# Performance work log

Hardware: AMD Instinct MI355X
Metric: run time of the kernel (lower is better)

Reference implementation:

```python
import jax, jax.numpy as jnp
import numpy as np

NEG_SLOPE = 0.2  # GATConv default negative_slope


def gat_conv(x, row, col, W, b, a_src, a_dst, N):
    # GATConv, heads=1, flow='target_to_source': i=row (central), j=col (neighbor)
    h = x @ W                                                   # [N, C]
    e = jax.nn.leaky_relu((h @ a_src)[col] + (h @ a_dst)[row], NEG_SLOPE)  # [E]
    m = jax.ops.segment_max(e, row, num_segments=N)             # segment softmax over row
    w = jnp.exp(e - m[row])
    denom = jax.ops.segment_sum(w, row, num_segments=N)
    alpha = w / (denom[row] + 1e-16)
    out = jax.ops.segment_sum(alpha[:, None] * h[col], row, num_segments=N)
    return out + b


def lstm_scan(xs_t, Wih, Whh, bih, bhh):
    # xs_t: [L, N, C] -> hidden states [L, N, H]; PyTorch gate order i,f,g,o
    H = Whh.shape[1]
    Nn = xs_t.shape[1]
    bias = bih + bhh
    def step(carry, xt):
        h, c = carry
        g = xt @ Wih.T + h @ Whh.T + bias
        i, f, gg, o = jnp.split(g, 4, axis=-1)
        c = jax.nn.sigmoid(f) * c + jax.nn.sigmoid(i) * jnp.tanh(gg)
        h = jax.nn.sigmoid(o) * jnp.tanh(c)
        return (h, c), h
    init = (jnp.zeros((Nn, H), xs_t.dtype), jnp.zeros((Nn, H), xs_t.dtype))
    _, hs = jax.lax.scan(step, init, xs_t)
    return hs


def jk_lstm(xst, Wih_f, Whh_f, bih_f, bhh_f, Wih_b, Whh_b, bih_b, bhh_b, att_W, att_b):
    # xst: [L, N, C]; bidirectional LSTM over layer dim, attention-weighted sum
    hf = lstm_scan(xst, Wih_f, Whh_f, bih_f, bhh_f)
    hb = lstm_scan(xst[::-1], Wih_b, Whh_b, bih_b, bhh_b)[::-1]
    h = jnp.concatenate([hf, hb], axis=-1)                      # [L, N, 2H]
    score = jnp.einsum('lnh,h->ln', h, att_W) + att_b           # [L, N]
    alpha = jax.nn.softmax(score, axis=0)                       # softmax over layers
    return jnp.einsum('lnc,ln->nc', xst, alpha)                 # [N, C]


def setup_inputs() -> dict:
    key = jax.random.key(0)
    ks = list(jax.random.split(key, 32))
    N, E, C = 50000, 800000, 128
    L = 3
    H = (L * C) // 2  # 192; PyG JumpingKnowledge lstm hidden size
    s = 0.05
    d = {}
    d['x'] = jax.random.normal(ks[0], (N, 3), jnp.float32)
    d['edge_index'] = jax.random.randint(ks[1], (2, E), 0, N, jnp.int64)
    d['gat_W0'] = jax.random.normal(ks[2], (3, C)) * 0.3
    d['gat_b0'] = jnp.zeros((C,))
    d['gat_as0'] = jax.random.normal(ks[3], (C,)) * s
    d['gat_ad0'] = jax.random.normal(ks[4], (C,)) * s
    d['gat_W'] = jax.random.normal(ks[5], (L - 1, C, C)) * s
    d['gat_b'] = jnp.zeros((L - 1, C))
    d['gat_as'] = jax.random.normal(ks[6], (L - 1, C)) * s
    d['gat_ad'] = jax.random.normal(ks[7], (L - 1, C)) * s
    d['lstm_Wih_f'] = jax.random.normal(ks[8], (4 * H, C)) * s
    d['lstm_Whh_f'] = jax.random.normal(ks[9], (4 * H, H)) * s
    d['lstm_bih_f'] = jnp.zeros((4 * H,))
    d['lstm_bhh_f'] = jnp.zeros((4 * H,))
    d['lstm_Wih_b'] = jax.random.normal(ks[10], (4 * H, C)) * s
    d['lstm_Whh_b'] = jax.random.normal(ks[11], (4 * H, H)) * s
    d['lstm_bih_b'] = jnp.zeros((4 * H,))
    d['lstm_bhh_b'] = jnp.zeros((4 * H,))
    d['att_W'] = jax.random.normal(ks[12], (2 * H,)) * s
    d['att_b'] = jnp.zeros((1,))
    d['nW1'] = jax.random.normal(ks[13], (C, C)) * s
    d['nb1'] = jnp.zeros((C,))
    d['nW2'] = jax.random.normal(ks[14], (C, 2)) * s
    d['nb2'] = jnp.zeros((2,))
    d['eW1'] = jax.random.normal(ks[15], (2 * C, C)) * s
    d['eb1'] = jnp.zeros((C,))
    d['eW2'] = jax.random.normal(ks[16], (C, 2)) * s
    d['eb2'] = jnp.zeros((2,))
    return d


def reference(x, edge_index, gat_W0, gat_b0, gat_as0, gat_ad0, gat_W, gat_b, gat_as, gat_ad,
              lstm_Wih_f, lstm_Whh_f, lstm_bih_f, lstm_bhh_f,
              lstm_Wih_b, lstm_Whh_b, lstm_bih_b, lstm_bhh_b,
              att_W, att_b, nW1, nb1, nW2, nb2, eW1, eb1, eW2, eb2):
    N = x.shape[0]
    row, col = edge_index[0], edge_index[1]
    xs = []
    h = jax.nn.relu(gat_conv(x, row, col, gat_W0, gat_b0, gat_as0, gat_ad0, N))
    xs.append(h)
    for l in range(gat_W.shape[0]):  # fixed small layer count
        h = jax.nn.relu(gat_conv(h, row, col, gat_W[l], gat_b[l], gat_as[l], gat_ad[l], N))
        xs.append(h)
    xst = jnp.stack(xs, axis=0)  # [L, N, C]
    h = jk_lstm(xst, lstm_Wih_f, lstm_Whh_f, lstm_bih_f, lstm_bhh_f,
                lstm_Wih_b, lstm_Whh_b, lstm_bih_b, lstm_bhh_b, att_W, att_b)
    # node classifier (dropout is identity in eval)
    node_out = jax.nn.softmax(jax.nn.relu(h @ nW1 + nb1) @ nW2 + nb2, axis=1)
    # edge representation gather + concat, then edge classifier
    edge_rep = jnp.concatenate([h[row], h[col]], axis=1)  # [E, 2C]
    edge_out = jax.nn.softmax(jax.nn.relu(edge_rep @ eW1 + eb1) @ eW2 + eb2, axis=1)
    return node_out, edge_out
```

## Files before the change

kernel.cpp:

```cpp
#include <hip/hip_runtime.h>
#include <cstdint>
#include <cstddef>


#define NIN 28
#define MAXJOBS 20

struct InPtrs { const void* p[NIN]; int n[NIN]; };

struct ConvJobs {
    const void* src[MAXJOBS];
    float* dst[MAXJOBS];
    int n[MAXJOBS];
    int ai[MAXJOBS];
    int blk0[MAXJOBS + 1];
    int njobs;
};

typedef short s16x4 __attribute__((ext_vector_type(4)));
typedef short s16x8 __attribute__((ext_vector_type(8)));
typedef float f32x4 __attribute__((ext_vector_type(4)));
typedef unsigned short u16x8 __attribute__((ext_vector_type(8)));

__device__ __forceinline__ float bf2f(unsigned short v) {
    unsigned int u = ((unsigned int)v) << 16;
    return __uint_as_float(u);
}

__device__ __forceinline__ unsigned short f2bf(float x) {
    unsigned int u = __float_as_uint(x);
    unsigned int r = u + 0x7fffu + ((u >> 16) & 1u);
    return (unsigned short)(r >> 16);
}

__device__ __forceinline__ float rdx(const void* p, size_t i, int isf32) {
    return isf32 ? ((const float*)p)[i] : bf2f(((const unsigned short*)p)[i]);
}

__device__ __forceinline__ float frcp(float x) {
    return __builtin_amdgcn_rcpf(x);
}

__device__ __forceinline__ float sigm(float x) {
    return frcp(1.f + __expf(-x));
}

__device__ __forceinline__ float fast_tanh(float x) {
    return 1.f - 2.f * frcp(__expf(2.f * x) + 1.f);
}

__global__ void k_sniff(InPtrs in, int* flags) {
    int ai = blockIdx.x;
    if (ai >= NIN) return;
    __shared__ int cnt;
    if (threadIdx.x == 0) cnt = 0;
    __syncthreads();
    if (ai == 1) {
        const int* w = (const int*)in.p[1];
        int nw = in.n[1] < 512 ? in.n[1] : 512;
        int local = 0;
        for (int i = threadIdx.x; i < nw; i += blockDim.x)
            if ((i & 1) && w[i] != 0) local++;
        atomicAdd(&cnt, local);
        __syncthreads();
        if (threadIdx.x == 0) flags[1] = (cnt < 4) ? 1 : 0;
        return;
    }
    const unsigned short* u = (const unsigned short*)in.p[ai];
    int ns = in.n[ai] < 256 ? in.n[ai] : 256;
    int local = 0;
    for (int i = threadIdx.x; i < ns; i += blockDim.x) {
        if (i & 1) continue;
        unsigned short v = u[i];
        int e = (v >> 7) & 0xff;
        if ((v & 0x7fff) != 0 && (e < 100 || e > 154)) local++;
    }
    atomicAdd(&cnt, local);
    __syncthreads();
    if (threadIdx.x == 0) flags[ai] = (cnt * 4 >= ns) ? 1 : 0;
}

__global__ void k_convall(ConvJobs J, const int* __restrict__ flags) {
    int b = blockIdx.x;
    int j = 0;
    while (j + 1 < J.njobs && b >= J.blk0[j + 1]) ++j;
    int i = (b - J.blk0[j]) * 256 + threadIdx.x;
    if (i >= J.n[j]) return;
    J.dst[j][i] = rdx(J.src[j], i, flags[J.ai[j]]);
}

__global__ void k_conve(const void* src, int* row, int* col, int E, const int* flags) {
    int i = blockIdx.x * blockDim.x + threadIdx.x;
    if (i >= E) return;
    if (flags[1]) {
        const long long* s = (const long long*)src;
        row[i] = (int)s[i];
        col[i] = (int)s[(size_t)E + i];
    } else {
        const int* s = (const int*)src;
        row[i] = s[i];
        col[i] = s[(size_t)E + i];
    }
}

__global__ void k_zeroi(int* p, int n) {
    int i = blockIdx.x * blockDim.x + threadIdx.x;
    if (i < n) p[i] = 0;
}

__global__ void k_hist(const int* __restrict__ row, int* __restrict__ cnt, int E) {
    int i = blockIdx.x * blockDim.x + threadIdx.x;
    if (i < E) atomicAdd(&cnt[row[i]], 1);
}

__global__ void k_scan1(const int* __restrict__ deg, int* __restrict__ indptr,
                        int* __restrict__ bsums, int N) {
    __shared__ int buf[1024];
    const int t = threadIdx.x;
    const int base = blockIdx.x * 1024;
    int v = (base + t < N) ? deg[base + t] : 0;
    buf[t] = v;
    __syncthreads();
    for (int ofs = 1; ofs < 1024; ofs <<= 1) {
        int add = (t >= ofs) ? buf[t - ofs] : 0;
        __syncthreads();
        buf[t] += add;
        __syncthreads();
    }
    if (base + t < N) indptr[base + t] = buf[t] - v;
    if (t == 1023) bsums[blockIdx.x] = buf[1023];
}

__global__ void k_scan2(int* bsums, int nb) {
    if (threadIdx.x == 0 && blockIdx.x == 0) {
        int acc = 0;
        for (int j = 0; j < nb; ++j) { int v = bsums[j]; bsums[j] = acc; acc += v; }
        bsums[nb] = acc;
    }
}

__global__ void k_scan3(const int* __restrict__ bsums, int* __restrict__ indptr,
                        int N, int nb) {
    int i = blockIdx.x * blockDim.x + threadIdx.x;
    if (i < N) indptr[i] += bsums[i >> 10];
    if (i == 0) indptr[N] = bsums[nb];
}

__global__ void k_fill(const int* __restrict__ row, const int* __restrict__ col,
                       const int* __restrict__ indptr, int* __restrict__ cur,
                       int* __restrict__ colS, int E) {
    int i = blockIdx.x * blockDim.x + threadIdx.x;
    if (i >= E) return;
    int r = row[i];
    int p = indptr[r] + atomicAdd(&cur[r], 1);
    colS[p] = col[i];
}

__global__ __launch_bounds__(256) void k_lin0(
    const float* __restrict__ x, const float* __restrict__ W0,
    const float* __restrict__ asrc, const float* __restrict__ adst,
    unsigned short* __restrict__ hlin, float* __restrict__ hs, float* __restrict__ hd,
    int N) {
    const int wid = threadIdx.x >> 6, lane = threadIdx.x & 63;
    const int n = blockIdx.x * 4 + wid;
    if (n >= N) return;
    float x0 = x[(size_t)n * 3], x1 = x[(size_t)n * 3 + 1], x2 = x[(size_t)n * 3 + 2];
    const int c0 = lane, c1 = lane + 64;
    float h0 = x0 * W0[c0] + x1 * W0[128 + c0] + x2 * W0[256 + c0];
    float h1 = x0 * W0[c1] + x1 * W0[128 + c1] + x2 * W0[256 + c1];
    hlin[(size_t)n * 128 + c0] = f2bf(h0);
    hlin[(size_t)n * 128 + c1] = f2bf(h1);
    float sp = h0 * asrc[c0] + h1 * asrc[c1];
    float dp = h0 * adst[c0] + h1 * adst[c1];
    for (int o = 32; o; o >>= 1) { sp += __shfl_down(sp, o); dp += __shfl_down(dp, o); }
    if (lane == 0) { hs[n] = sp; hd[n] = dp; }
}

__global__ __launch_bounds__(256) void k_lin(
    const unsigned short* __restrict__ xin, const float* __restrict__ W,
    const float* __restrict__ asrc, const float* __restrict__ adst,
    unsigned short* __restrict__ hlin, float* __restrict__ hs, float* __restrict__ hd,
    int N) {
    __shared__ float xl[16][128];
    const int t = threadIdx.x;
    const int wid = t >> 6, lane = t & 63;
    const int nb = blockIdx.x * 16;
    for (int i = t; i < 2048; i += 256) {
        int r = i >> 7, k = i & 127;
        int n = nb + r;
        xl[r][k] = (n < N) ? bf2f(xin[(size_t)n * 128 + k]) : 0.f;
    }
    __syncthreads();
    const int c0 = lane, c1 = lane + 64;
    const int r0 = wid * 4;
    float h0[4], h1[4];
    #pragma unroll
    for (int j = 0; j < 4; ++j) { h0[j] = 0.f; h1[j] = 0.f; }
    #pragma unroll 2
    for (int k = 0; k < 128; ++k) {
        float w0 = W[k * 128 + c0], w1 = W[k * 128 + c1];
        #pragma unroll
        for (int j = 0; j < 4; ++j) {
            float xv = xl[r0 + j][k];
            h0[j] += xv * w0;
            h1[j] += xv * w1;
        }
    }
    float sp[4], dp[4];
    #pragma unroll
    for (int j = 0; j < 4; ++j) {
        sp[j] = h0[j] * asrc[c0] + h1[j] * asrc[c1];
        dp[j] = h0[j] * adst[c0] + h1[j] * adst[c1];
    }
    #pragma unroll
    for (int o = 32; o; o >>= 1) {
        #pragma unroll
        for (int j = 0; j < 4; ++j) {
            sp[j] += __shfl_down(sp[j], o);
            dp[j] += __shfl_down(dp[j], o);
        }
    }
    #pragma unroll
    for (int j = 0; j < 4; ++j) {
        int n = nb + r0 + j;
        if (n < N) {
            hlin[(size_t)n * 128 + c0] = f2bf(h0[j]);
            hlin[(size_t)n * 128 + c1] = f2bf(h1[j]);
            if (lane == 0) { hs[n] = sp[j]; hd[n] = dp[j]; }
        }
    }
}

__global__ __launch_bounds__(256) void k_aggr(
    const unsigned short* __restrict__ hlin, const float* __restrict__ hs,
    const float* __restrict__ hd,
    const int* __restrict__ indptr, const int* __restrict__ colS,
    const float* __restrict__ b, unsigned short* __restrict__ xout, int N) {
    const int wid = threadIdx.x >> 6, lane = threadIdx.x & 63;
    const int n = blockIdx.x * 4 + wid;
    if (n >= N) return;
    const int s = indptr[n], epos = indptr[n + 1];
    const float hdv = hd[n];
    const int c0 = lane, c1 = lane + 64;
    float m = -1e30f, d = 0.f, a0 = 0.f, a1 = 0.f;
    int idx = s;
    for (; idx + 8 <= epos; idx += 8) {
        int cl[8];
        #pragma unroll
        for (int j = 0; j < 8; ++j) cl[j] = colS[idx + j];
        float e[8];
        #pragma unroll
        for (int j = 0; j < 8; ++j) {
            float ev = hs[cl[j]] + hdv;
            e[j] = (ev > 0.f) ? ev : 0.2f * ev;
        }
        float v0[8], v1[8];
        #pragma unroll
        for (int j = 0; j < 8; ++j) {
            const unsigned short* hp = hlin + (size_t)cl[j] * 128;
            v0[j] = bf2f(hp[c0]);
            v1[j] = bf2f(hp[c1]);
        }
        float m8 = e[0];
        #pragma unroll
        for (int j = 1; j < 8; ++j) m8 = fmaxf(m8, e[j]);
        if (m8 > m) {
            float sc = __expf(m - m8);
            a0 *= sc; a1 *= sc; d *= sc; m = m8;
        }
        #pragma unroll
        for (int j = 0; j < 8; ++j) {
            float w = __expf(e[j] - m);
            a0 += w * v0[j];
            a1 += w * v1[j];
            d  += w;
        }
    }
    for (; idx < epos; ++idx) {
        int col = colS[idx];
        float e = hs[col] + hdv;
        e = (e > 0.f) ? e : 0.2f * e;
        const unsigned short* hr = hlin + (size_t)col * 128;
        float v0 = bf2f(hr[c0]), v1 = bf2f(hr[c1]);
        if (e > m) {
            float sc = __expf(m - e);
            a0 = a0 * sc + v0;
            a1 = a1 * sc + v1;
            d  = d * sc + 1.f;
            m  = e;
        } else {
            float w = __expf(e - m);
            a0 += w * v0;
            a1 += w * v1;
            d  += w;
        }
    }
    float inv = frcp(d + 1e-16f);
    float r0 = a0 * inv + b[c0];
    float r1 = a1 * inv + b[c1];
    xout[(size_t)n * 128 + c0] = f2bf(fmaxf(r0, 0.f));
    xout[(size_t)n * 128 + c1] = f2bf(fmaxf(r1, 0.f));
}

__global__ void k_wpack(const void* Wihf, const void* Whhf,
                        const void* Wihb, const void* Whhb,
                        const void* bihf, const void* bhhf,
                        const void* bihb, const void* bhhb,
                        const int* __restrict__ flags,
                        unsigned short* __restrict__ Bpack, float* __restrict__ bsum) {
    int idx = blockIdx.x * blockDim.x + threadIdx.x;
    const int TOT = 2 * 10 * 48 * 512;
    if (idx < TOT) {
        int dir = idx / (10 * 48 * 512);
        int r   = idx % (10 * 48 * 512);
        int kb  = r / (48 * 512);
        int r2  = r % (48 * 512);
        int f   = r2 / 512;
        int q   = r2 % 512;
        int lane = q >> 3, j = q & 7;
        int k   = kb * 32 + ((j >> 2) * 16) + ((lane >> 4) * 4) + (j & 3);
        int col = f * 16 + (lane & 15);
        float v;
        if (k < 128)
            v = dir ? rdx(Wihb, (size_t)col * 128 + k, flags[14])
                    : rdx(Wihf, (size_t)col * 128 + k, flags[10]);
        else
            v = dir ? rdx(Whhb, (size_t)col * 192 + (k - 128), flags[15])
                    : rdx(Whhf, (size_t)col * 192 + (k - 128), flags[11]);
        Bpack[idx] = f2bf(v);
    }
    if (idx < 2 * 768) {
        int d = idx / 768, j = idx % 768;
        bsum[idx] = d ? rdx(bihb, j, flags[16]) + rdx(bhhb, j, flags[17])
                      : rdx(bihf, j, flags[12]) + rdx(bhhf, j, flags[13]);
    }
}

__global__ __launch_bounds__(768, 3) void k_lstm_mfma(
    const unsigned short* __restrict__ xsb,
    const unsigned short* __restrict__ Bpack,
    const float* __restrict__ bsum,
    const float* __restrict__ attW,
    float* __restrict__ scoreP,
    int N) {
    __shared__ unsigned short AS[64][332];
    __shared__ float scoreS[64];
    const int t = threadIdx.x;
    const int bf = t >> 6, lane = t & 63;
    const int dir = blockIdx.y;
    const int n0 = blockIdx.x * 64;
    const int ccol = lane & 15;
    const int klane = lane >> 4;
    const int lrow = klane * 4;
    const int akl = klane * 4;
    const int m = bf * 16 + ccol;

    const float bI = bsum[dir * 768 + m];
    const float bF = bsum[dir * 768 + 192 + m];
    const float bG = bsum[dir * 768 + 384 + m];
    const float bO = bsum[dir * 768 + 576 + m];
    const float awt = attW[dir * 192 + m];
    float cst[16];
    #pragma unroll
    for (int i = 0; i < 16; ++i) cst[i] = 0.f;

    const unsigned short* Bd = Bpack + (size_t)dir * 10 * 48 * 512;

    for (int s = 0; s < 3; ++s) {
        const int l = dir ? (2 - s) : s;
        {
            const unsigned short* xsrc = xsb + ((size_t)l * N + n0) * 128;
            for (int i = t; i < 1024; i += 768) {
                int r = i >> 4, kq = (i & 15) * 8;
                u16x8 v = (u16x8)(0);
                if (n0 + r < N) v = *(const u16x8*)(xsrc + (size_t)r * 128 + kq);
                *(u16x8*)&AS[r][kq] = v;
            }
        }
        if (t < 64) scoreS[t] = 0.f;
        __syncthreads();

        const int KB = s ? 10 : 4;
        f32x4 acc[4][4];
        #pragma unroll
        for (int rf = 0; rf < 4; ++rf)
            #pragma unroll
            for (int g = 0; g < 4; ++g) acc[rf][g] = (f32x4)(0.f);
        s16x8 bA[4], bB[4];
        {
            const unsigned short* bb = Bd + (size_t)bf * 512 + lane * 8;
            #pragma unroll
            for (int g = 0; g < 4; ++g) bA[g] = *(const s16x8*)(bb + (size_t)g * 6144);
        }
        for (int kb = 0; kb < KB; kb += 2) {
            {
                const unsigned short* bb = Bd + ((size_t)(kb + 1) * 48 + bf) * 512 + lane * 8;
                #pragma unroll
                for (int g = 0; g < 4; ++g) bB[g] = *(const s16x8*)(bb + (size_t)g * 6144);
            }
            {
                const int k0 = kb * 32 + akl;
                s16x8 av[4];
                #pragma unroll
                for (int rf = 0; rf < 4; ++rf) {
                    s16x4 alo = *(const s16x4*)&AS[rf * 16 + ccol][k0];
                    s16x4 ahi = *(const s16x4*)&AS[rf * 16 + ccol][k0 + 16];
                    av[rf] = __builtin_shufflevector(alo, ahi, 0, 1, 2, 3, 4, 5, 6, 7);
                }
                #pragma unroll
                for (int rf = 0; rf < 4; ++rf)
                    #pragma unroll
                    for (int g = 0; g < 4; ++g)
                        acc[rf][g] = __builtin_amdgcn_mfma_f32_16x16x32_bf16(
                            av[rf], bA[g], acc[rf][g], 0, 0, 0);
            }
            if (kb + 2 < KB) {
                const unsigned short* bb = Bd + ((size_t)(kb + 2) * 48 + bf) * 512 + lane * 8;
                #pragma unroll
                for (int g = 0; g < 4; ++g) bA[g] = *(const s16x8*)(bb + (size_t)g * 6144);
            }
            {
                const int k0 = (kb + 1) * 32 + akl;
                s16x8 av[4];
                #pragma unroll
                for (int rf = 0; rf < 4; ++rf) {
                    s16x4 alo = *(const s16x4*)&AS[rf * 16 + ccol][k0];
                    s16x4 ahi = *(const s16x4*)&AS[rf * 16 + ccol][k0 + 16];
                    av[rf] = __builtin_shufflevector(alo, ahi, 0, 1, 2, 3, 4, 5, 6, 7);
                }
                #pragma unroll
                for (int rf = 0; rf < 4; ++rf)
                    #pragma unroll
                    for (int g = 0; g < 4; ++g)
                        acc[rf][g] = __builtin_amdgcn_mfma_f32_16x16x32_bf16(
                            av[rf], bB[g], acc[rf][g], 0, 0, 0);
            }
        }
        __syncthreads();

        float sp[16];
        #pragma unroll
        for (int rf = 0; rf < 4; ++rf) {
            #pragma unroll
            for (int reg = 0; reg < 4; ++reg) {
                float gI = acc[rf][0][reg] + bI;
                float gF = acc[rf][1][reg] + bF;
                float gG = acc[rf][2][reg] + bG;
                float gO = acc[rf][3][reg] + bO;
                float ig = sigm(gI);
                float fg = sigm(gF);
                float gt = fast_tanh(gG);
                float og = sigm(gO);
                int ci = rf * 4 + reg;
                float cn = fg * cst[ci] + ig * gt;
                cst[ci] = cn;
                float hh = og * fast_tanh(cn);
                AS[rf * 16 + lrow + reg][128 + m] = f2bf(hh);
                sp[ci] = hh * awt;
            }
        }
        #pragma unroll
        for (int o = 1; o < 16; o <<= 1) {
            #pragma unroll
            for (int i = 0; i < 16; ++i) sp[i] += __shfl_xor(sp[i], o);
        }
        if (ccol == 0) {
            #pragma unroll
            for (int i = 0; i < 16; ++i)
                atomicAdd(&scoreS[(i >> 2) * 16 + lrow + (i & 3)], sp[i]);
        }
        __syncthreads();
        if (t < 64 && n0 + t < N)
            scoreP[(size_t)(dir * 3 + l) * N + n0 + t] = scoreS[t];
    }
}

__global__ __launch_bounds__(256) void k_tail(
    const unsigned short* __restrict__ xsb, const float* __restrict__ scoreP,
    const float* __restrict__ nW1, const float* __restrict__ nb1,
    const float* __restrict__ nW2, const float* __restrict__ nb2,
    const float* __restrict__ eW1, const float* __restrict__ eb1,
    unsigned short* __restrict__ P, unsigned short* __restrict__ Q,
    float* __restrict__ out, int N) {
    __shared__ float xl[16][128];
    __shared__ float al[16][4];
    const int t = threadIdx.x;
    const int wid = t >> 6, lane = t & 63;
    const int nb = blockIdx.x * 16;
    if (t < 16) {
        int n = nb + t;
        float e0 = 0.f, e1 = 0.f, e2 = 0.f;
        if (n < N) {
            float s0 = scoreP[n]                 + scoreP[(size_t)3 * N + n];
            float s1 = scoreP[(size_t)N + n]     + scoreP[(size_t)4 * N + n];
            float s2 = scoreP[(size_t)2 * N + n] + scoreP[(size_t)5 * N + n];
            float mm = fmaxf(s0, fmaxf(s1, s2));
            e0 = __expf(s0 - mm); e1 = __expf(s1 - mm); e2 = __expf(s2 - mm);
            float inv = frcp(e0 + e1 + e2);
            e0 *= inv; e1 *= inv; e2 *= inv;
        }
        al[t][0] = e0; al[t][1] = e1; al[t][2] = e2;
    }
    __syncthreads();
    const size_t L1o = (size_t)N * 128, L2o = 2 * L1o;
    for (int i = t; i < 2048; i += 256) {
        int r = i >> 7, k = i & 127;
        int n = nb + r;
        float v = 0.f;
        if (n < N) {
            size_t p = (size_t)n * 128 + k;
            v = al[r][0] * bf2f(xsb[p]) + al[r][1] * bf2f(xsb[L1o + p])
              + al[r][2] * bf2f(xsb[L2o + p]);
        }
        xl[r][k] = v;
    }
    __syncthreads();
    const int c0 = lane, c1 = lane + 64;
    const int r0 = wid * 4;
    {
        float h0[4], h1[4];
        #pragma unroll
        for (int j = 0; j < 4; ++j) { h0[j] = 0.f; h1[j] = 0.f; }
        #pragma unroll 2
        for (int k = 0; k < 128; ++k) {
            float w0 = nW1[k * 128 + c0], w1 = nW1[k * 128 + c1];
            #pragma unroll
            for (int j = 0; j < 4; ++j) {
                float xv = xl[r0 + j][k];
                h0[j] += xv * w0;
                h1[j] += xv * w1;
            }
        }
        float p0[4], p1[4];
        #pragma unroll
        for (int j = 0; j < 4; ++j) {
            float a = fmaxf(h0[j] + nb1[c0], 0.f);
            float bq = fmaxf(h1[j] + nb1[c1], 0.f);
            p0[j] = a * nW2[c0 * 2 + 0] + bq * nW2[c1 * 2 + 0];
            p1[j] = a * nW2[c0 * 2 + 1] + bq * nW2[c1 * 2 + 1];
        }
        #pragma unroll
        for (int o = 32; o; o >>= 1) {
            #pragma unroll
            for (int j = 0; j < 4; ++j) {
                p0[j] += __shfl_down(p0[j], o);
                p1[j] += __shfl_down(p1[j], o);
            }
        }
        if (lane == 0) {
            #pragma unroll
            for (int j = 0; j < 4; ++j) {
                int n = nb + r0 + j;
                if (n < N) {
                    float l0 = p0[j] + nb2[0], l1 = p1[j] + nb2[1];
                    float mm = fmaxf(l0, l1);
                    float e0 = __expf(l0 - mm), e1 = __expf(l1 - mm);
                    float inv = frcp(e0 + e1);
                    out[2 * (size_t)n]     = e0 * inv;
                    out[2 * (size_t)n + 1] = e1 * inv;
                }
            }
        }
    }
    {
        float pp0[4], pp1[4], qq0[4], qq1[4];
        #pragma unroll
        for (int j = 0; j < 4; ++j) { pp0[j] = 0.f; pp1[j] = 0.f; qq0[j] = 0.f; qq1[j] = 0.f; }
        for (int k = 0; k < 128; ++k) {
            float wp0 = eW1[k * 128 + c0], wp1 = eW1[k * 128 + c1];
            float wq0 = eW1[(128 + k) * 128 + c0], wq1 = eW1[(128 + k) * 128 + c1];
            #pragma unroll
            for (int j = 0; j < 4; ++j) {
                float xv = xl[r0 + j][k];
                pp0[j] += xv * wp0; pp1[j] += xv * wp1;
                qq0[j] += xv * wq0; qq1[j] += xv * wq1;
            }
        }
        #pragma unroll
        for (int j = 0; j < 4; ++j) {
            int n = nb + r0 + j;
            if (n < N) {
                P[(size_t)n * 128 + c0] = f2bf(pp0[j] + eb1[c0]);
                P[(size_t)n * 128 + c1] = f2bf(pp1[j] + eb1[c1]);
                Q[(size_t)n * 128 + c0] = f2bf(qq0[j]);
                Q[(size_t)n * 128 + c1] = f2bf(qq1[j]);
            }
        }
    }
}

__global__ __launch_bounds__(256) void k_edge2(
    const unsigned short* __restrict__ P, const unsigned short* __restrict__ Q,
    const int* __restrict__ row, const int* __restrict__ col,
    const float* __restrict__ W2, const float* __restrict__ b2,
    float* __restrict__ out, long long E, int N) {
    long long g = (((long long)blockIdx.x * blockDim.x) + threadIdx.x) >> 4;
    const int sl = threadIdx.x & 15;
    if (g >= E) return;
    int r = row[g], c = col[g];
    u16x8 pv = *(const u16x8*)(P + (size_t)r * 128 + sl * 8);
    u16x8 qv = *(const u16x8*)(Q + (size_t)c * 128 + sl * 8);
    const float4* w2 = (const float4*)W2 + sl * 4;
    float l0 = 0.f, l1 = 0.f;
    #pragma unroll
    for (int jj = 0; jj < 4; ++jj) {
        float h0 = fmaxf(bf2f(pv[2 * jj])     + bf2f(qv[2 * jj]), 0.f);
        float h1 = fmaxf(bf2f(pv[2 * jj + 1]) + bf2f(qv[2 * jj + 1]), 0.f);
        float4 wv = w2[jj];
        l0 += h0 * wv.x + h1 * wv.z;
        l1 += h0 * wv.y + h1 * wv.w;
    }
    #pragma unroll
    for (int o = 1; o < 16; o <<= 1) { l0 += __shfl_xor(l0, o); l1 += __shfl_xor(l1, o); }
    if (sl == 0) {
        l0 += b2[0]; l1 += b2[1];
        float mm = fmaxf(l0, l1);
        float e0 = __expf(l0 - mm), e1 = __expf(l1 - mm);
        float inv = frcp(e0 + e1);
        out[2 * (long long)N + 2 * g]     = e0 * inv;
        out[2 * (long long)N + 2 * g + 1] = e1 * inv;
    }
}

extern "C" void kernel_launch(void* const* d_in, const int* in_sizes, int n_in,
                              void* d_out, int out_size, void* d_ws, size_t ws_size,
                              hipStream_t stream) {
    if (n_in < NIN) return;
    const int N = in_sizes[0] / 3;
    const int E = in_sizes[1] / 2;

    char* ws = (char*)d_ws;
    size_t off = 0;
    auto alloc = [&](size_t bytes) -> char* {
        char* p = ws + off;
        off = (off + bytes + 255) & ~(size_t)255;
        return p;
    };
    int* flags = (int*)alloc(32 * sizeof(int));
    int* bsums = (int*)alloc(128 * sizeof(int));
    float* canon[NIN];
    for (int i = 0; i < NIN; ++i) canon[i] = nullptr;
    for (int i = 0; i < NIN; ++i) {
        if (i == 1 || (i >= 10 && i <= 17)) continue;
        canon[i] = (float*)alloc((size_t)in_sizes[i] * 4);
    }
    int* row32  = (int*)alloc((size_t)E * 4);
    int* col32  = (int*)alloc((size_t)E * 4);
    int* indptr = (int*)alloc((size_t)(N + 1) * 4);
    int* cnt    = (int*)alloc((size_t)N * 4);
    int* colS   = (int*)alloc((size_t)E * 4);
    float* hs   = (float*)alloc((size_t)N * 4);
    float* hd   = (float*)alloc((size_t)N * 4);
    float* hJK  = (float*)alloc((size_t)N * 128 * 4);
    unsigned short* hlin = (unsigned short*)hJK;
    unsigned short* xsb = (unsigned short*)alloc((size_t)3 * N * 128 * 2);
    unsigned short* Bpack = (unsigned short*)alloc((size_t)2 * 10 * 48 * 512 * 2);
    float* bsum = (float*)alloc((size_t)2 * 768 * 4);
    float* scoreP;
    if ((size_t)E >= (size_t)6 * N) scoreP = (float*)colS;
    else                            scoreP = (float*)alloc((size_t)6 * N * 4);
    if (off > ws_size) return;
    unsigned short* P = (unsigned short*)hJK;
    unsigned short* Q = (unsigned short*)hJK + (size_t)N * 128;

    InPtrs ip;
    for (int i = 0; i < NIN; ++i) { ip.p[i] = d_in[i]; ip.n[i] = in_sizes[i]; }

    k_sniff<<<NIN, 256, 0, stream>>>(ip, flags);

    {
        ConvJobs J;
        int nj = 0, blk = 0;
        for (int i = 0; i < NIN; ++i) {
            if (i == 1 || (i >= 10 && i <= 17)) continue;
            J.src[nj] = d_in[i];
            J.dst[nj] = canon[i];
            J.n[nj] = in_sizes[i];
            J.ai[nj] = i;
            J.blk0[nj] = blk;
            blk += (in_sizes[i] + 255) / 256;
            ++nj;
        }
        J.blk0[nj] = blk;
        J.njobs = nj;
        k_convall<<<blk, 256, 0, stream>>>(J, flags);
    }
    k_conve<<<(E + 255) / 256, 256, 0, stream>>>(d_in[1], row32, col32, E, flags);
    k_wpack<<<(2 * 10 * 48 * 512 + 255) / 256, 256, 0, stream>>>(
        d_in[10], d_in[11], d_in[14], d_in[15],
        d_in[12], d_in[13], d_in[16], d_in[17], flags, Bpack, bsum);

    const int nb1k = (N + 1023) / 1024;
    k_zeroi<<<(N + 255) / 256, 256, 0, stream>>>(cnt, N);
    k_hist<<<(E + 255) / 256, 256, 0, stream>>>(row32, cnt, E);
    k_scan1<<<nb1k, 1024, 0, stream>>>(cnt, indptr, bsums, N);
    k_scan2<<<1, 64, 0, stream>>>(bsums, nb1k);
    k_scan3<<<(N + 255) / 256, 256, 0, stream>>>(bsums, indptr, N, nb1k);
    k_zeroi<<<(N + 255) / 256, 256, 0, stream>>>(cnt, N);
    k_fill<<<(E + 255) / 256, 256, 0, stream>>>(row32, col32, indptr, cnt, colS, E);

    k_lin0<<<(N + 3) / 4, 256, 0, stream>>>(canon[0], canon[2], canon[4], canon[5],
                                            hlin, hs, hd, N);
    k_aggr<<<(N + 3) / 4, 256, 0, stream>>>(hlin, hs, hd, indptr, colS, canon[3], xsb, N);
    for (int l = 1; l < 3; ++l) {
        const float* W  = canon[6] + (size_t)(l - 1) * 128 * 128;
        const float* bb = canon[7] + (size_t)(l - 1) * 128;
        const float* as = canon[8] + (size_t)(l - 1) * 128;
        const float* ad = canon[9] + (size_t)(l - 1) * 128;
        k_lin<<<(N + 15) / 16, 256, 0, stream>>>(xsb + (size_t)(l - 1) * N * 128, W, as, ad,
                                                 hlin, hs, hd, N);
        k_aggr<<<(N + 3) / 4, 256, 0, stream>>>(hlin, hs, hd, indptr, colS, bb,
                                                xsb + (size_t)l * N * 128, N);
    }

    dim3 lgrid((N + 63) / 64, 2);
    k_lstm_mfma<<<lgrid, 768, 0, stream>>>(xsb, Bpack, bsum, canon[18], scoreP, N);

    float* out = (float*)d_out;
    k_tail<<<(N + 15) / 16, 256, 0, stream>>>(xsb, scoreP,
                                              canon[20], canon[21], canon[22], canon[23],
                                              canon[24], canon[25], P, Q, out, N);
    {
        long long tot = (long long)E * 16;
        int blocks = (int)((tot + 255) / 256);
        k_edge2<<<blocks, 256, 0, stream>>>(P, Q, row32, col32, canon[26], canon[27],
                                            out, (long long)E, N);
    }
}
```

Before: 709.8 us.

## Process edges per CSR row to reuse source projection, drop atomics

The edge classifier is restructured to walk the CSR by source node, one wavefront per node. Each node's P row is loaded once and reused across all its edges, and two edges are processed per iteration. An edge-index permutation array is now recorded during CSR fill so outputs can be scattered back to their original edge order. Separately, the LSTM score reduction replaces shared-memory atomics with per-wavefront slots summed afterward, and the zero kernels become hipMemsetAsync. The cost is an extra E-sized index array, scattered output writes, and load imbalance across rows with different degrees.

```diff
diff --git a/kernel.cpp b/kernel.cpp
--- a/kernel.cpp
+++ b/kernel.cpp
@@ -103,11 +103,6 @@
     }
 }
 
-__global__ void k_zeroi(int* p, int n) {
-    int i = blockIdx.x * blockDim.x + threadIdx.x;
-    if (i < n) p[i] = 0;
-}
-
 __global__ void k_hist(const int* __restrict__ row, int* __restrict__ cnt, int E) {
     int i = blockIdx.x * blockDim.x + threadIdx.x;
     if (i < E) atomicAdd(&cnt[row[i]], 1);
@@ -148,12 +143,13 @@
 
 __global__ void k_fill(const int* __restrict__ row, const int* __restrict__ col,
                        const int* __restrict__ indptr, int* __restrict__ cur,
-                       int* __restrict__ colS, int E) {
+                       int* __restrict__ colS, int* __restrict__ eidx, int E) {
     int i = blockIdx.x * blockDim.x + threadIdx.x;
     if (i >= E) return;
     int r = row[i];
     int p = indptr[r] + atomicAdd(&cur[r], 1);
     colS[p] = col[i];
+    eidx[p] = i;
 }
 
 __global__ __launch_bounds__(256) void k_lin0(
@@ -344,7 +340,7 @@
     float* __restrict__ scoreP,
     int N) {
     __shared__ unsigned short AS[64][332];
-    __shared__ float scoreS[64];
+    __shared__ float scoreW[12][64];
     const int t = threadIdx.x;
     const int bf = t >> 6, lane = t & 63;
     const int dir = blockIdx.y;
@@ -377,7 +373,6 @@
                 *(u16x8*)&AS[r][kq] = v;
             }
         }
-        if (t < 64) scoreS[t] = 0.f;
         __syncthreads();
 
         const int KB = s ? 10 : 4;
@@ -467,11 +462,15 @@
         if (ccol == 0) {
             #pragma unroll
             for (int i = 0; i < 16; ++i)
-                atomicAdd(&scoreS[(i >> 2) * 16 + lrow + (i & 3)], sp[i]);
+                scoreW[bf][(i >> 2) * 16 + lrow + (i & 3)] = sp[i];
         }
         __syncthreads();
-        if (t < 64 && n0 + t < N)
-            scoreP[(size_t)(dir * 3 + l) * N + n0 + t] = scoreS[t];
+        if (t < 64 && n0 + t < N) {
+            float ss = 0.f;
+            #pragma unroll
+            for (int b2 = 0; b2 < 12; ++b2) ss += scoreW[b2][t];
+            scoreP[(size_t)(dir * 3 + l) * N + n0 + t] = ss;
+        }
     }
 }
 
@@ -589,36 +588,76 @@
     }
 }
 
-__global__ __launch_bounds__(256) void k_edge2(
+__global__ __launch_bounds__(256) void k_edge3(
     const unsigned short* __restrict__ P, const unsigned short* __restrict__ Q,
-    const int* __restrict__ row, const int* __restrict__ col,
+    const int* __restrict__ indptr, const int* __restrict__ colS,
+    const int* __restrict__ eidx,
     const float* __restrict__ W2, const float* __restrict__ b2,
-    float* __restrict__ out, long long E, int N) {
-    long long g = (((long long)blockIdx.x * blockDim.x) + threadIdx.x) >> 4;
-    const int sl = threadIdx.x & 15;
-    if (g >= E) return;
-    int r = row[g], c = col[g];
-    u16x8 pv = *(const u16x8*)(P + (size_t)r * 128 + sl * 8);
-    u16x8 qv = *(const u16x8*)(Q + (size_t)c * 128 + sl * 8);
-    const float4* w2 = (const float4*)W2 + sl * 4;
-    float l0 = 0.f, l1 = 0.f;
-    #pragma unroll
-    for (int jj = 0; jj < 4; ++jj) {
-        float h0 = fmaxf(bf2f(pv[2 * jj])     + bf2f(qv[2 * jj]), 0.f);
-        float h1 = fmaxf(bf2f(pv[2 * jj + 1]) + bf2f(qv[2 * jj + 1]), 0.f);
-        float4 wv = w2[jj];
-        l0 += h0 * wv.x + h1 * wv.z;
-        l1 += h0 * wv.y + h1 * wv.w;
-    }
-    #pragma unroll
-    for (int o = 1; o < 16; o <<= 1) { l0 += __shfl_xor(l0, o); l1 += __shfl_xor(l1, o); }
-    if (sl == 0) {
-        l0 += b2[0]; l1 += b2[1];
-        float mm = fmaxf(l0, l1);
-        float e0 = __expf(l0 - mm), e1 = __expf(l1 - mm);
-        float inv = frcp(e0 + e1);
-        out[2 * (long long)N + 2 * g]     = e0 * inv;
-        out[2 * (long long)N + 2 * g + 1] = e1 * inv;
+    float* __restrict__ out, int N) {
+    const int wid = threadIdx.x >> 6, lane = threadIdx.x & 63;
+    const int n = blockIdx.x * 4 + wid;
+    if (n >= N) return;
+    const int sl = lane & 15, g = lane >> 4;
+    const int s = indptr[n], e = indptr[n + 1];
+    float pf[8];
+    {
+        u16x8 pv = *(const u16x8*)(P + (size_t)n * 128 + sl * 8);
+        #pragma unroll
+        for (int j = 0; j < 8; ++j) pf[j] = bf2f(pv[j]);
+    }
+    float w2v[8];
+    {
+        const float4* w2 = (const float4*)W2 + sl * 4;
+        #pragma unroll
+        for (int jj = 0; jj < 4; ++jj) {
+            float4 wv = w2[jj];
+            w2v[2 * jj]     = wv.x;
+            w2v[2 * jj + 1] = wv.z;
+        }
+    }
+    const float* W2f = W2;
+    const float b20 = b2[0], b21 = b2[1];
+    for (int p = s + g; p < e; p += 8) {
+        int p1 = p + 4;
+        bool v1 = p1 < e;
+        int col0 = colS[p],  eo0 = eidx[p];
+        int col1 = v1 ? colS[p1] : col0;
+        int eo1  = v1 ? eidx[p1] : 0;
+        u16x8 qv0 = *(const u16x8*)(Q + (size_t)col0 * 128 + sl * 8);
+        u16x8 qv1 = *(const u16x8*)(Q + (size_t)col1 * 128 + sl * 8);
+        float l00 = 0.f, l01 = 0.f, l10 = 0.f, l11 = 0.f;
+        #pragma unroll
+        for (int j = 0; j < 8; ++j) {
+            int ch = sl * 8 + j;
+            float wA = W2f[ch * 2], wB = W2f[ch * 2 + 1];
+            float h0 = fmaxf(pf[j] + bf2f(qv0[j]), 0.f);
+            float h1 = fmaxf(pf[j] + bf2f(qv1[j]), 0.f);
+            l00 += h0 * wA; l01 += h0 * wB;
+            l10 += h1 * wA; l11 += h1 * wB;
+        }
+        #pragma unroll
+        for (int o = 1; o < 16; o <<= 1) {
+            l00 += __shfl_xor(l00, o); l01 += __shfl_xor(l01, o);
+            l10 += __shfl_xor(l10, o); l11 += __shfl_xor(l11, o);
+        }
+        if (sl == 0) {
+            {
+                float a = l00 + b20, b = l01 + b21;
+                float mm = fmaxf(a, b);
+                float e0 = __expf(a - mm), e1 = __expf(b - mm);
+                float inv = frcp(e0 + e1);
+                out[2 * (size_t)N + 2 * (size_t)eo0]     = e0 * inv;
+                out[2 * (size_t)N + 2 * (size_t)eo0 + 1] = e1 * inv;
+            }
+            if (v1) {
+                float a = l10 + b20, b = l11 + b21;
+                float mm = fmaxf(a, b);
+                float e0 = __expf(a - mm), e1 = __expf(b - mm);
+                float inv = frcp(e0 + e1);
+                out[2 * (size_t)N + 2 * (size_t)eo1]     = e0 * inv;
+                out[2 * (size_t)N + 2 * (size_t)eo1 + 1] = e1 * inv;
+            }
+        }
     }
 }
 
@@ -649,6 +688,7 @@
     int* indptr = (int*)alloc((size_t)(N + 1) * 4);
     int* cnt    = (int*)alloc((size_t)N * 4);
     int* colS   = (int*)alloc((size_t)E * 4);
+    int* eidx   = (int*)alloc((size_t)E * 4);
     float* hs   = (float*)alloc((size_t)N * 4);
     float* hd   = (float*)alloc((size_t)N * 4);
     float* hJK  = (float*)alloc((size_t)N * 128 * 4);
@@ -656,9 +696,7 @@
     unsigned short* xsb = (unsigned short*)alloc((size_t)3 * N * 128 * 2);
     unsigned short* Bpack = (unsigned short*)alloc((size_t)2 * 10 * 48 * 512 * 2);
     float* bsum = (float*)alloc((size_t)2 * 768 * 4);
-    float* scoreP;
-    if ((size_t)E >= (size_t)6 * N) scoreP = (float*)colS;
-    else                            scoreP = (float*)alloc((size_t)6 * N * 4);
+    float* scoreP = (float*)alloc((size_t)6 * N * 4);
     if (off > ws_size) return;
     unsigned short* P = (unsigned short*)hJK;
     unsigned short* Q = (unsigned short*)hJK + (size_t)N * 128;
@@ -691,13 +729,13 @@
         d_in[12], d_in[13], d_in[16], d_in[17], flags, Bpack, bsum);
 
     const int nb1k = (N + 1023) / 1024;
-    k_zeroi<<<(N + 255) / 256, 256, 0, stream>>>(cnt, N);
+    hipMemsetAsync(cnt, 0, (size_t)N * 4, stream);
     k_hist<<<(E + 255) / 256, 256, 0, stream>>>(row32, cnt, E);
     k_scan1<<<nb1k, 1024, 0, stream>>>(cnt, indptr, bsums, N);
     k_scan2<<<1, 64, 0, stream>>>(bsums, nb1k);
     k_scan3<<<(N + 255) / 256, 256, 0, stream>>>(bsums, indptr, N, nb1k);
-    k_zeroi<<<(N + 255) / 256, 256, 0, stream>>>(cnt, N);
-    k_fill<<<(E + 255) / 256, 256, 0, stream>>>(row32, col32, indptr, cnt, colS, E);
+    hipMemsetAsync(cnt, 0, (size_t)N * 4, stream);
+    k_fill<<<(E + 255) / 256, 256, 0, stream>>>(row32, col32, indptr, cnt, colS, eidx, E);
 
     k_lin0<<<(N + 3) / 4, 256, 0, stream>>>(canon[0], canon[2], canon[4], canon[5],
                                             hlin, hs, hd, N);
@@ -720,10 +758,6 @@
     k_tail<<<(N + 15) / 16, 256, 0, stream>>>(xsb, scoreP,
                                               canon[20], canon[21], canon[22], canon[23],
                                               canon[24], canon[25], P, Q, out, N);
-    {
-        long long tot = (long long)E * 16;
-        int blocks = (int)((tot + 255) / 256);
-        k_edge2<<<blocks, 256, 0, stream>>>(P, Q, row32, col32, canon[26], canon[27],
-                                            out, (long long)E, N);
-    }
-}
+    k_edge3<<<(N + 3) / 4, 256, 0, stream>>>(P, Q, indptr, colS, eidx,
+                                             canon[26], canon[27], out, N);
+}
```

Result: no change. 716.7 us (+1.0%).
